# Kernel optimization log

Measured on AMD Instinct MI355X. Metric: run time of the kernel, lower is better.

## Reference

```python
import jax, jax.numpy as jnp
import numpy as np

N = 50000
E = 600000
NODE_DIM = 128
EDGE_DIM = 16
HID = 128


def _tconv(x, src, dst, ea, Wq, bq, Wk, bk, Wv, bv, We, be, Ws, bs, heads, C, concat):
    """PyG TransformerConv (root_weight=True, beta=False), eval mode (no dropout)."""
    n = x.shape[0]
    q = (x @ Wq + bq).reshape(n, heads, C)[dst]          # [E,H,C] query at target
    k = (x @ Wk + bk).reshape(n, heads, C)[src]          # [E,H,C] key at source
    v = (x @ Wv + bv).reshape(n, heads, C)[src]          # [E,H,C] value at source
    e = (ea @ We + be).reshape(-1, heads, C)             # [E,H,C] edge embedding
    k = k + e
    score = (q * k).sum(-1) / jnp.sqrt(jnp.asarray(C, x.dtype))  # [E,H]
    # segment softmax over incoming edges of each target node
    m = jax.ops.segment_max(score, dst, num_segments=n)
    m = jnp.where(jnp.isfinite(m), m, jnp.zeros_like(m))  # nodes w/o in-edges
    ex = jnp.exp(score - m[dst])
    den = jax.ops.segment_sum(ex, dst, num_segments=n)
    alpha = ex / (den[dst] + 1e-16)                       # [E,H]
    msg = (v + e) * alpha[..., None]                      # [E,H,C]
    out = jax.ops.segment_sum(msg, dst, num_segments=n)   # [N,H,C]
    out = out.reshape(n, heads * C) if concat else out.mean(axis=1)
    return out + x @ Ws + bs                              # root skip connection


def setup_inputs() -> dict:
    key = jax.random.key(0)
    ks = jax.random.split(key, 32)
    d = {
        "x": jax.random.normal(ks[0], (N, NODE_DIM), jnp.float32),
        "ei": jax.random.randint(ks[1], (2, E), 0, N, jnp.int32),
        "ea": jax.random.normal(ks[2], (E, EDGE_DIM), jnp.float32),
    }
    H1, C1 = 8, HID // 8
    def w(k, shape):
        return jax.random.normal(k, shape, jnp.float32) * 0.05
    # layer 1: in=NODE_DIM, heads=8, out=HID//8, concat=True
    d["Wq1"] = w(ks[3], (NODE_DIM, H1 * C1)); d["bq1"] = jnp.zeros((H1 * C1,), jnp.float32)
    d["Wk1"] = w(ks[4], (NODE_DIM, H1 * C1)); d["bk1"] = jnp.zeros((H1 * C1,), jnp.float32)
    d["Wv1"] = w(ks[5], (NODE_DIM, H1 * C1)); d["bv1"] = jnp.zeros((H1 * C1,), jnp.float32)
    d["We1"] = w(ks[6], (EDGE_DIM, H1 * C1)); d["be1"] = jnp.zeros((H1 * C1,), jnp.float32)
    d["Ws1"] = w(ks[7], (NODE_DIM, H1 * C1)); d["bs1"] = jnp.zeros((H1 * C1,), jnp.float32)
    # layer 2: in=HID, heads=1, out=HID, concat=False -> skip maps to HID
    d["Wq2"] = w(ks[8], (HID, HID)); d["bq2"] = jnp.zeros((HID,), jnp.float32)
    d["Wk2"] = w(ks[9], (HID, HID)); d["bk2"] = jnp.zeros((HID,), jnp.float32)
    d["Wv2"] = w(ks[10], (HID, HID)); d["bv2"] = jnp.zeros((HID,), jnp.float32)
    d["We2"] = w(ks[11], (EDGE_DIM, HID)); d["be2"] = jnp.zeros((HID,), jnp.float32)
    d["Ws2"] = w(ks[12], (HID, HID)); d["bs2"] = jnp.zeros((HID,), jnp.float32)
    return d


def reference(x, ei, ea,
              Wq1, bq1, Wk1, bk1, Wv1, bv1, We1, be1, Ws1, bs1,
              Wq2, bq2, Wk2, bk2, Wv2, bv2, We2, be2, Ws2, bs2):
    src, dst = ei[0], ei[1]
    h = _tconv(x, src, dst, ea, Wq1, bq1, Wk1, bk1, Wv1, bv1, We1, be1, Ws1, bs1,
               heads=8, C=HID // 8, concat=True)
    h = jax.nn.leaky_relu(h, negative_slope=0.01)
    # dropout is identity in eval mode
    out = _tconv(h, src, dst, ea, Wq2, bq2, Wk2, bk2, Wv2, bv2, We2, be2, Ws2, bs2,
                 heads=1, C=HID, concat=False)
    return out
```

## Files before the change

### kernel.cpp

```cpp
#include <hip/hip_runtime.h>
#include <math.h>

typedef __bf16 bf16x8 __attribute__((ext_vector_type(8)));
typedef float f32x4 __attribute__((ext_vector_type(4)));

__device__ __forceinline__ unsigned short f2bf(float f) {
    unsigned u = __float_as_uint(f);
    return (unsigned short)((u + 0x7fffu + ((u >> 16) & 1u)) >> 16);
}
__device__ __forceinline__ float2 bf2(unsigned u) {
    float2 r;
    r.x = __uint_as_float(u << 16);
    r.y = __uint_as_float(u & 0xffff0000u);
    return r;
}

__global__ __launch_bounds__(256) void convert_x(
    const float* __restrict__ x, unsigned short* __restrict__ xb, int total)
{
    int g = blockIdx.x * blockDim.x + threadIdx.x;
    if (g < total) xb[g] = f2bf(x[g]);
}

__global__ __launch_bounds__(256) void prep_w(
    const float* __restrict__ Wq, const float* __restrict__ bq,
    const float* __restrict__ Wk, const float* __restrict__ bk,
    const float* __restrict__ Wv, const float* __restrict__ bv,
    const float* __restrict__ be,
    const float* __restrict__ Ws, const float* __restrict__ bs,
    const float* __restrict__ We, int H,
    unsigned short* __restrict__ Wt, float* __restrict__ bias)
{
    int g = blockIdx.x * blockDim.x + threadIdx.x;
    const int C = 128 / H;
    if (g < 640) {
        int p = g;
        float b;
        if (p < 256) {
            int cc = 2 * (p >> 2) + (p & 1);
            b = ((p & 2) ? bv[cc] : bk[cc]) + be[cc];
        }
        else if (p < 384) b = bq[p - 256];
        else if (p < 512) b = bs[p - 384];
        else {
            int c2 = p - 512, h = c2 >> 4, kk = c2 & 15;
            b = 0.f;
            if (h < H) for (int i = 0; i < C; ++i) b += bq[h * C + i] * We[kk * 128 + h * C + i];
        }
        bias[p] = b;
    }
    if (g >= 640 * 128) return;
    int p = g >> 7, d = g & 127;
    float w;
    if (p < 256) {
        int cc = 2 * (p >> 2) + (p & 1);
        w = (p & 2) ? Wv[d * 128 + cc] : Wk[d * 128 + cc];
    } else if (p < 384) {
        w = Wq[d * 128 + (p - 256)];
    } else if (p < 512) {
        w = Ws[d * 128 + (p - 384)];
    } else {
        int c2 = p - 512, h = c2 >> 4, kk = c2 & 15;
        w = 0.f;
        if (h < H) for (int i = 0; i < C; ++i) w += Wq[d * 128 + h * C + i] * We[kk * 128 + h * C + i];
    }
    Wt[(size_t)p * 128 + d] = f2bf(w);
}

__global__ __launch_bounds__(256) void gemm_bf16(
    const unsigned short* __restrict__ Xb, int M,
    const unsigned short* __restrict__ Wt, const float* __restrict__ bias,
    unsigned short* __restrict__ P, float* __restrict__ qWe)
{
    __shared__ unsigned short Bs[64][136];
    __shared__ unsigned short tile[4][16][64];
    const int wv = threadIdx.x >> 6, lane = threadIdx.x & 63;
    const int row0 = blockIdx.x * 64 + wv * 16;
    const int n0 = blockIdx.y * 64;
    const int quad = lane >> 4, l16 = lane & 15;

    {
        const uint4* gsrc = (const uint4*)(Wt + (size_t)n0 * 128);
#pragma unroll
        for (int u = 0; u < 4; ++u) {
            int v = threadIdx.x + u * 256;
            int col = v >> 4, k8 = v & 15;
            *(uint4*)(&Bs[col][k8 * 8]) = gsrc[v];
        }
    }
    __syncthreads();

    f32x4 acc[4] = {};
    int mrow = row0 + l16; if (mrow >= M) mrow = M - 1;
    const int kb = quad * 8;
#pragma unroll
    for (int kk = 0; kk < 4; ++kk) {
        bf16x8 a = *(const bf16x8*)(Xb + (size_t)mrow * 128 + kk * 32 + kb);
#pragma unroll
        for (int f = 0; f < 4; ++f) {
            bf16x8 b = *(const bf16x8*)(&Bs[f * 16 + l16][kk * 32 + kb]);
            acc[f] = __builtin_amdgcn_mfma_f32_16x16x32_bf16(a, b, acc[f], 0, 0, 0);
        }
    }
    if (n0 < 512) {
#pragma unroll
        for (int f = 0; f < 4; ++f) {
            float bs = bias[n0 + f * 16 + l16];
#pragma unroll
            for (int r = 0; r < 4; ++r) {
                int row = quad * 4 + r;
                int col = f * 16 + l16;
                tile[wv][row][col ^ ((row & 3) << 4)] = f2bf(acc[f][r] + bs);
            }
        }
        __syncthreads();
        int row = lane >> 2, seg = lane & 3;
        int m = row0 + row;
        if (m < M) {
            const uint4* src = (const uint4*)&tile[wv][row][(seg ^ (row & 3)) << 4];
            uint4* dst = (uint4*)(P + (size_t)m * 512 + n0 + seg * 16);
            dst[0] = src[0];
            dst[1] = src[1];
        }
    } else {
#pragma unroll
        for (int f = 0; f < 4; ++f) {
            int c = n0 + f * 16 + l16;
            float bs = bias[c];
#pragma unroll
            for (int r = 0; r < 4; ++r) {
                int m = row0 + quad * 4 + r;
                if (m < M) qWe[(size_t)m * 128 + (c - 512)] = acc[f][r] + bs;
            }
        }
    }
}

__global__ __launch_bounds__(256) void degree_kernel(
    const int* __restrict__ ei, int* __restrict__ deg, int E)
{
    int e = blockIdx.x * blockDim.x + threadIdx.x;
    if (e < E) atomicAdd(&deg[ei[E + e]], 1);
}

__global__ __launch_bounds__(256) void scan_part1(
    const int* __restrict__ deg, int* __restrict__ partial, int N)
{
    __shared__ int s[256];
    const int t = threadIdx.x;
    const int g = blockIdx.x * 256 + t;
    int v = (g < N) ? deg[g] : 0;
    s[t] = v;
    __syncthreads();
    for (int ofs = 128; ofs > 0; ofs >>= 1) {
        if (t < ofs) s[t] += s[t + ofs];
        __syncthreads();
    }
    if (t == 0) partial[blockIdx.x] = s[0];
}

__global__ __launch_bounds__(256) void scan_part2(
    int* __restrict__ partial)
{
    __shared__ int s[256];
    const int t = threadIdx.x;
    int v = partial[t];
    s[t] = v;
    __syncthreads();
    for (int ofs = 1; ofs < 256; ofs <<= 1) {
        int u = (t >= ofs) ? s[t - ofs] : 0;
        __syncthreads();
        s[t] += u;
        __syncthreads();
    }
    partial[t] = s[t] - v;
}

__global__ __launch_bounds__(256) void scan_part3(
    const int* __restrict__ deg, const int* __restrict__ offs,
    int* __restrict__ rowptr, int* __restrict__ cursor, int N)
{
    __shared__ int s[256];
    const int t = threadIdx.x;
    const int g = blockIdx.x * 256 + t;
    int v = (g < N) ? deg[g] : 0;
    s[t] = v;
    __syncthreads();
    for (int ofs = 1; ofs < 256; ofs <<= 1) {
        int u = (t >= ofs) ? s[t - ofs] : 0;
        __syncthreads();
        s[t] += u;
        __syncthreads();
    }
    const int incl = s[t];
    const int base = offs[blockIdx.x];
    if (g < N) {
        cursor[g] = base + incl - v;
        rowptr[g + 1] = base + incl;
    }
    if (g == 0) rowptr[0] = 0;
}

__global__ __launch_bounds__(256) void scatter_kernel(
    const int* __restrict__ ei, int* __restrict__ cursor,
    int2* __restrict__ csr, int E)
{
    int e = blockIdx.x * blockDim.x + threadIdx.x;
    if (e < E) {
        int pos = atomicAdd(&cursor[ei[E + e]], 1);
        csr[pos] = make_int2(ei[e], e);
    }
}

__global__ __launch_bounds__(256) void fused1_node(
    const unsigned short* __restrict__ P, const float* __restrict__ qWe,
    const float* __restrict__ ea, const float* __restrict__ We1,
    const int2* __restrict__ csr, const int* __restrict__ rowptr,
    unsigned short* __restrict__ h1, int N)
{
    const int lane = threadIdx.x & 63;
    const int node = blockIdx.x * 8 + (threadIdx.x >> 5);
    if (node >= N) return;
    const int l32 = lane & 31;
    const int hbit = lane & 32;
    const int sub4 = l32 & 3;
    const int c0 = l32 * 4;
    const int hsrc = hbit | (l32 & 28);

    const int beg = rowptr[node];
    const int deg = rowptr[node + 1] - beg;

    uint2 su = *(const uint2*)(P + (size_t)node * 512 + 384 + c0);
    float2 ska = bf2(su.x), skb = bf2(su.y);
    if (deg == 0) {
        float o0 = ska.x > 0.f ? ska.x : 0.01f * ska.x;
        float o1 = ska.y > 0.f ? ska.y : 0.01f * ska.y;
        float o2 = skb.x > 0.f ? skb.x : 0.01f * skb.x;
        float o3 = skb.y > 0.f ? skb.y : 0.01f * skb.y;
        uint2 pk;
        pk.x = (unsigned)f2bf(o0) | ((unsigned)f2bf(o1) << 16);
        pk.y = (unsigned)f2bf(o2) | ((unsigned)f2bf(o3) << 16);
        *(uint2*)(h1 + (size_t)node * 128 + c0) = pk;
        return;
    }

    uint2 qu = *(const uint2*)(P + (size_t)node * 512 + 256 + c0);
    float2 qa = bf2(qu.x), qb = bf2(qu.y);
    float4 qw4 = *(const float4*)(qWe + (size_t)node * 128 + c0);

    float4 acc = make_float4(0.f, 0.f, 0.f, 0.f);
    float4 A2  = make_float4(0.f, 0.f, 0.f, 0.f);
    float m = -INFINITY, lden = 0.f;

    int2 se = make_int2(0, 0);
    if (l32 < deg) se = csr[beg + l32];

    for (int blk = 0; blk < deg; blk += 32) {
        if (blk) se = (blk + l32 < deg) ? csr[beg + blk + l32] : make_int2(0, 0);
        const int bcnt = min(32, deg - blk);
        for (int cb = 0; cb < bcnt; cb += 8) {
            const int lim = min(8, bcnt - cb);
            uint4 kv[8]; float4 ea4[8];
#pragma unroll
            for (int i = 0; i < 8; ++i) {
                if (i < lim) {
                    int jc = min(cb + i, bcnt - 1);
                    int sb = __shfl(se.x, hbit | jc, 64);
                    int eb = __shfl(se.y, hbit | jc, 64);
                    kv[i]  = *(const uint4*)(P + (size_t)sb * 512 + l32 * 8);
                    ea4[i] = *(const float4*)(ea + (size_t)eb * 16 + sub4 * 4);
                }
            }
            float s0 = -INFINITY, s1 = -INFINITY;
#pragma unroll
            for (int i = 0; i < 8; ++i) {
                if (i < lim) {
                    float2 ka = bf2(kv[i].x), kb = bf2(kv[i].z);
                    float p = qa.x * ka.x + qa.y * ka.y + qb.x * kb.x + qb.y * kb.y
                            + qw4.x * ea4[i].x + qw4.y * ea4[i].y
                            + qw4.z * ea4[i].z + qw4.w * ea4[i].w;
                    p += __shfl_xor(p, 1, 64);
                    p += __shfl_xor(p, 2, 64);
                    float pv = p * 0.25f;
                    if (sub4 == (i & 3)) { if (i < 4) s0 = pv; else s1 = pv; }
                }
            }
            float cm = fmaxf(s0, s1);
            cm = fmaxf(cm, __shfl_xor(cm, 1, 64));
            cm = fmaxf(cm, __shfl_xor(cm, 2, 64));
            float m_new = fmaxf(m, cm);
            float scale = __expf(m - m_new);
            float e0 = __expf(s0 - m_new);
            float e1 = __expf(s1 - m_new);
            float ds = e0 + e1;
            ds += __shfl_xor(ds, 1, 64);
            ds += __shfl_xor(ds, 2, 64);
            lden = lden * scale + ds;
            acc.x *= scale; acc.y *= scale; acc.z *= scale; acc.w *= scale;
            A2.x  *= scale; A2.y  *= scale; A2.z  *= scale; A2.w  *= scale;
            m = m_new;
#pragma unroll
            for (int i = 0; i < 8; ++i) {
                if (i < lim) {
                    float w = __shfl((i < 4) ? e0 : e1, hsrc | (i & 3), 64);
                    float2 va = bf2(kv[i].y), vb = bf2(kv[i].w);
                    acc.x += w * va.x; acc.y += w * va.y;
                    acc.z += w * vb.x; acc.w += w * vb.y;
                    A2.x += w * ea4[i].x; A2.y += w * ea4[i].y;
                    A2.z += w * ea4[i].z; A2.w += w * ea4[i].w;
                }
            }
        }
    }

    float ex0 = 0.f, ex1 = 0.f, ex2 = 0.f, ex3 = 0.f;
#pragma unroll
    for (int k = 0; k < 16; ++k) {
        float comp = (k & 3) == 0 ? A2.x : (k & 3) == 1 ? A2.y : (k & 3) == 2 ? A2.z : A2.w;
        float ak = __shfl(comp, hsrc | (k >> 2), 64);
        float4 w4 = *(const float4*)(We1 + k * 128 + c0);
        ex0 += ak * w4.x; ex1 += ak * w4.y; ex2 += ak * w4.z; ex3 += ak * w4.w;
    }
    float inv = 1.f / (lden + 1e-16f);
    float o0 = (acc.x + ex0) * inv + ska.x;
    float o1 = (acc.y + ex1) * inv + ska.y;
    float o2 = (acc.z + ex2) * inv + skb.x;
    float o3 = (acc.w + ex3) * inv + skb.y;
    o0 = o0 > 0.f ? o0 : 0.01f * o0;
    o1 = o1 > 0.f ? o1 : 0.01f * o1;
    o2 = o2 > 0.f ? o2 : 0.01f * o2;
    o3 = o3 > 0.f ? o3 : 0.01f * o3;
    uint2 pk;
    pk.x = (unsigned)f2bf(o0) | ((unsigned)f2bf(o1) << 16);
    pk.y = (unsigned)f2bf(o2) | ((unsigned)f2bf(o3) << 16);
    *(uint2*)(h1 + (size_t)node * 128 + c0) = pk;
}

__global__ __launch_bounds__(256) void fused2_node(
    const unsigned short* __restrict__ P, const float* __restrict__ qWe,
    const float* __restrict__ ea, const float* __restrict__ We2,
    const int2* __restrict__ csr, const int* __restrict__ rowptr,
    float* __restrict__ out, int N)
{
    const int lane = threadIdx.x & 63;
    const int node = blockIdx.x * 8 + (threadIdx.x >> 5);
    if (node >= N) return;
    const int l32 = lane & 31;
    const int hbit = lane & 32;
    const int c0 = l32 * 4;
    const int k16 = lane & 15;

    const int beg = rowptr[node];
    const int deg = rowptr[node + 1] - beg;

    uint2 su = *(const uint2*)(P + (size_t)node * 512 + 384 + c0);
    float2 ska = bf2(su.x), skb = bf2(su.y);
    float* outp = out + (size_t)node * 128 + c0;
    if (deg == 0) {
        *(float4*)outp = make_float4(ska.x, ska.y, skb.x, skb.y);
        return;
    }

    uint2 qu = *(const uint2*)(P + (size_t)node * 512 + 256 + c0);
    float2 qa = bf2(qu.x), qb = bf2(qu.y);
    float qw = qWe[(size_t)node * 128 + k16];

    float4 acc = make_float4(0.f, 0.f, 0.f, 0.f);
    float accA = 0.f;
    float m = -INFINITY, lden = 0.f;

    int2 se = make_int2(0, 0);
    if (l32 < deg) se = csr[beg + l32];

    for (int blk = 0; blk < deg; blk += 32) {
        if (blk) se = (blk + l32 < deg) ? csr[beg + blk + l32] : make_int2(0, 0);
        const int bcnt = min(32, deg - blk);
        for (int cb = 0; cb < bcnt; cb += 8) {
            const int lim = min(8, bcnt - cb);
            uint4 kv[8]; float eav[8];
#pragma unroll
            for (int i = 0; i < 8; ++i) {
                if (i < lim) {
                    int jc = min(cb + i, bcnt - 1);
                    int sb = __shfl(se.x, hbit | jc, 64);
                    int eb = __shfl(se.y, hbit | jc, 64);
                    kv[i]  = *(const uint4*)(P + (size_t)sb * 512 + l32 * 8);
                    eav[i] = ea[(size_t)eb * 16 + k16];
                }
            }
            float my_s = -INFINITY;
#pragma unroll
            for (int i = 0; i < 8; ++i) {
                if (i < lim) {
                    float2 ka = bf2(kv[i].x), kb = bf2(kv[i].z);
                    float p = qa.x * ka.x + qa.y * ka.y + qb.x * kb.x + qb.y * kb.y
                            + 0.5f * qw * eav[i];
                    p += __shfl_xor(p, 1, 64);
                    p += __shfl_xor(p, 2, 64);
                    p += __shfl_xor(p, 4, 64);
                    p += __shfl_xor(p, 8, 64);
                    p += __shfl_xor(p, 16, 64);
                    if (l32 == i) my_s = p * 0.08838834764831845f;
                }
            }
            float cm = my_s;
#pragma unroll
            for (int mk = 1; mk < 32; mk <<= 1) cm = fmaxf(cm, __shfl_xor(cm, mk, 64));
            float m_new = fmaxf(m, cm);
            float scale = __expf(m - m_new);
            float ew = __expf(my_s - m_new);
            float ds = ew;
#pragma unroll
            for (int mk = 1; mk < 32; mk <<= 1) ds += __shfl_xor(ds, mk, 64);
            lden = lden * scale + ds;
            acc.x *= scale; acc.y *= scale; acc.z *= scale; acc.w *= scale;
            accA *= scale;
            m = m_new;
#pragma unroll
            for (int i = 0; i < 8; ++i) {
                if (i < lim) {
                    float w = __shfl(ew, hbit | i, 64);
                    float2 va = bf2(kv[i].y), vb = bf2(kv[i].w);
                    acc.x += w * va.x; acc.y += w * va.y;
                    acc.z += w * vb.x; acc.w += w * vb.y;
                    accA += w * eav[i];
                }
            }
        }
    }

    float ex0 = 0.f, ex1 = 0.f, ex2 = 0.f, ex3 = 0.f;
#pragma unroll
    for (int k = 0; k < 16; ++k) {
        float ak = __shfl(accA, hbit | k, 64);
        float4 w4 = *(const float4*)(We2 + k * 128 + c0);
        ex0 += ak * w4.x; ex1 += ak * w4.y; ex2 += ak * w4.z; ex3 += ak * w4.w;
    }
    float inv = 1.f / (lden + 1e-16f);
    float4 o;
    o.x = (acc.x + ex0) * inv + ska.x;
    o.y = (acc.y + ex1) * inv + ska.y;
    o.z = (acc.z + ex2) * inv + skb.x;
    o.w = (acc.w + ex3) * inv + skb.y;
    *(float4*)outp = o;
}

extern "C" void kernel_launch(void* const* d_in, const int* in_sizes, int n_in,
                              void* d_out, int out_size, void* d_ws, size_t ws_size,
                              hipStream_t stream)
{
    const float* x  = (const float*)d_in[0];
    const int*   ei = (const int*)d_in[1];
    const float* ea = (const float*)d_in[2];
    const float *Wq1 = (const float*)d_in[3],  *bq1 = (const float*)d_in[4];
    const float *Wk1 = (const float*)d_in[5],  *bk1 = (const float*)d_in[6];
    const float *Wv1 = (const float*)d_in[7],  *bv1 = (const float*)d_in[8];
    const float *We1 = (const float*)d_in[9],  *be1 = (const float*)d_in[10];
    const float *Ws1 = (const float*)d_in[11], *bs1 = (const float*)d_in[12];
    const float *Wq2 = (const float*)d_in[13], *bq2 = (const float*)d_in[14];
    const float *Wk2 = (const float*)d_in[15], *bk2 = (const float*)d_in[16];
    const float *Wv2 = (const float*)d_in[17], *bv2 = (const float*)d_in[18];
    const float *We2 = (const float*)d_in[19], *be2 = (const float*)d_in[20];
    const float *Ws2 = (const float*)d_in[21], *bs2 = (const float*)d_in[22];

    const int N = in_sizes[0] / 128;
    const int E = in_sizes[1] / 2;

    char* ws = (char*)d_ws;
    size_t off = 0;
    auto alloc = [&](size_t bytes) -> void* {
        void* p = ws + off;
        off = (off + bytes + 255) & ~(size_t)255;
        return p;
    };
    unsigned short* xb  = (unsigned short*)alloc((size_t)N * 128 * 2);
    unsigned short* P   = (unsigned short*)alloc((size_t)N * 512 * 2);
    unsigned short* h1b = (unsigned short*)alloc((size_t)N * 128 * 2);
    unsigned short* Wt1 = (unsigned short*)alloc((size_t)640 * 128 * 2);
    unsigned short* Wt2 = (unsigned short*)alloc((size_t)640 * 128 * 2);
    float* bias1 = (float*)alloc(640 * 4);
    float* bias2 = (float*)alloc(640 * 4);
    float* qWe   = (float*)alloc((size_t)N * 128 * 4);
    int*  deg    = (int*)alloc((size_t)N * 4);
    int*  rowptr = (int*)alloc((size_t)(N + 1) * 4);
    int*  cursor = (int*)alloc((size_t)N * 4);
    int*  partial= (int*)alloc(256 * 4);
    int2* csr    = (int2*)alloc((size_t)E * 8);

    dim3 gemm_grid1((N + 63) / 64, 10);
    dim3 gemm_grid2((N + 63) / 64, 9);
    const int tn = N * 128;
    const int node_blocks = (N + 7) / 8;
    const int prep_blocks = (640 * 128 + 255) / 256;
    const int scan_blocks = (N + 255) / 256;

    convert_x<<<(tn + 255) / 256, 256, 0, stream>>>(x, xb, tn);
    prep_w<<<prep_blocks, 256, 0, stream>>>(Wq1, bq1, Wk1, bk1, Wv1, bv1, be1, Ws1, bs1, We1, 8, Wt1, bias1);
    prep_w<<<prep_blocks, 256, 0, stream>>>(Wq2, bq2, Wk2, bk2, Wv2, bv2, be2, Ws2, bs2, We2, 1, Wt2, bias2);

    hipMemsetAsync(deg, 0, (size_t)N * 4, stream);
    hipMemsetAsync(partial, 0, 256 * 4, stream);
    degree_kernel<<<(E + 255) / 256, 256, 0, stream>>>(ei, deg, E);
    scan_part1<<<scan_blocks, 256, 0, stream>>>(deg, partial, N);
    scan_part2<<<1, 256, 0, stream>>>(partial);
    scan_part3<<<scan_blocks, 256, 0, stream>>>(deg, partial, rowptr, cursor, N);
    scatter_kernel<<<(E + 255) / 256, 256, 0, stream>>>(ei, cursor, csr, E);

    gemm_bf16<<<gemm_grid1, 256, 0, stream>>>(xb, N, Wt1, bias1, P, qWe);
    fused1_node<<<node_blocks, 256, 0, stream>>>(P, qWe, ea, We1, csr, rowptr, h1b, N);

    gemm_bf16<<<gemm_grid2, 256, 0, stream>>>(h1b, N, Wt2, bias2, P, qWe);
    fused2_node<<<node_blocks, 256, 0, stream>>>(P, qWe, ea, We2, csr, rowptr, (float*)d_out, N);
}
```

Before: 498.4 us.

## Use 16 lanes per node in fused attention kernels, 8 channels per lane

Both fused node kernels now map each destination node to 16 lanes instead of 32, with every lane handling 8 channels through two 16-byte loads. The aim is fewer shuffle-reduction steps per edge, wider vector loads, and twice as many nodes per block so uneven degrees leave fewer lanes idle. In exchange, each lane holds more registers for key/value and edge-feature tiles. The edge batch per iteration also shrinks from 8 to 4, which lowers memory-level parallelism per node.

```diff
diff --git a/kernel.cpp b/kernel.cpp
--- a/kernel.cpp
+++ b/kernel.cpp
@@ -219,121 +219,159 @@
     unsigned short* __restrict__ h1, int N)
 {
     const int lane = threadIdx.x & 63;
-    const int node = blockIdx.x * 8 + (threadIdx.x >> 5);
+    const int node = blockIdx.x * 16 + (threadIdx.x >> 4);
     if (node >= N) return;
-    const int l32 = lane & 31;
-    const int hbit = lane & 32;
-    const int sub4 = l32 & 3;
-    const int c0 = l32 * 4;
-    const int hsrc = hbit | (l32 & 28);
+    const int l16 = lane & 15;
+    const int qbit = lane & 48;
+    const int pbit = lane & 62;
+    const int odd  = lane & 1;
+    const int c0 = l16 * 8;
 
     const int beg = rowptr[node];
     const int deg = rowptr[node + 1] - beg;
 
-    uint2 su = *(const uint2*)(P + (size_t)node * 512 + 384 + c0);
-    float2 ska = bf2(su.x), skb = bf2(su.y);
+    uint4 su = *(const uint4*)(P + (size_t)node * 512 + 384 + c0);
+    float2 sk0 = bf2(su.x), sk1 = bf2(su.y), sk2 = bf2(su.z), sk3 = bf2(su.w);
     if (deg == 0) {
-        float o0 = ska.x > 0.f ? ska.x : 0.01f * ska.x;
-        float o1 = ska.y > 0.f ? ska.y : 0.01f * ska.y;
-        float o2 = skb.x > 0.f ? skb.x : 0.01f * skb.x;
-        float o3 = skb.y > 0.f ? skb.y : 0.01f * skb.y;
-        uint2 pk;
+        float o0 = sk0.x > 0.f ? sk0.x : 0.01f * sk0.x;
+        float o1 = sk0.y > 0.f ? sk0.y : 0.01f * sk0.y;
+        float o2 = sk1.x > 0.f ? sk1.x : 0.01f * sk1.x;
+        float o3 = sk1.y > 0.f ? sk1.y : 0.01f * sk1.y;
+        float o4 = sk2.x > 0.f ? sk2.x : 0.01f * sk2.x;
+        float o5 = sk2.y > 0.f ? sk2.y : 0.01f * sk2.y;
+        float o6 = sk3.x > 0.f ? sk3.x : 0.01f * sk3.x;
+        float o7 = sk3.y > 0.f ? sk3.y : 0.01f * sk3.y;
+        uint4 pk;
         pk.x = (unsigned)f2bf(o0) | ((unsigned)f2bf(o1) << 16);
         pk.y = (unsigned)f2bf(o2) | ((unsigned)f2bf(o3) << 16);
-        *(uint2*)(h1 + (size_t)node * 128 + c0) = pk;
+        pk.z = (unsigned)f2bf(o4) | ((unsigned)f2bf(o5) << 16);
+        pk.w = (unsigned)f2bf(o6) | ((unsigned)f2bf(o7) << 16);
+        *(uint4*)(h1 + (size_t)node * 128 + c0) = pk;
         return;
     }
 
-    uint2 qu = *(const uint2*)(P + (size_t)node * 512 + 256 + c0);
-    float2 qa = bf2(qu.x), qb = bf2(qu.y);
-    float4 qw4 = *(const float4*)(qWe + (size_t)node * 128 + c0);
-
-    float4 acc = make_float4(0.f, 0.f, 0.f, 0.f);
-    float4 A2  = make_float4(0.f, 0.f, 0.f, 0.f);
+    uint4 qu = *(const uint4*)(P + (size_t)node * 512 + 256 + c0);
+    float2 q0 = bf2(qu.x), q1 = bf2(qu.y), q2 = bf2(qu.z), q3 = bf2(qu.w);
+    float4 qwA = *(const float4*)(qWe + (size_t)node * 128 + c0);
+    float4 qwB = *(const float4*)(qWe + (size_t)node * 128 + c0 + 4);
+
+    float4 acA = make_float4(0.f, 0.f, 0.f, 0.f);
+    float4 acB = make_float4(0.f, 0.f, 0.f, 0.f);
+    float4 A2a = make_float4(0.f, 0.f, 0.f, 0.f);
+    float4 A2b = make_float4(0.f, 0.f, 0.f, 0.f);
     float m = -INFINITY, lden = 0.f;
 
     int2 se = make_int2(0, 0);
-    if (l32 < deg) se = csr[beg + l32];
-
-    for (int blk = 0; blk < deg; blk += 32) {
-        if (blk) se = (blk + l32 < deg) ? csr[beg + blk + l32] : make_int2(0, 0);
-        const int bcnt = min(32, deg - blk);
-        for (int cb = 0; cb < bcnt; cb += 8) {
-            const int lim = min(8, bcnt - cb);
-            uint4 kv[8]; float4 ea4[8];
-#pragma unroll
-            for (int i = 0; i < 8; ++i) {
+    if (l16 < deg) se = csr[beg + l16];
+
+    for (int blk = 0; blk < deg; blk += 16) {
+        if (blk) se = (blk + l16 < deg) ? csr[beg + blk + l16] : make_int2(0, 0);
+        const int bcnt = min(16, deg - blk);
+        for (int cb = 0; cb < bcnt; cb += 4) {
+            const int lim = min(4, bcnt - cb);
+            uint4 kva[4], kvb[4]; float4 eaA[4], eaB[4];
+#pragma unroll
+            for (int i = 0; i < 4; ++i) {
                 if (i < lim) {
                     int jc = min(cb + i, bcnt - 1);
-                    int sb = __shfl(se.x, hbit | jc, 64);
-                    int eb = __shfl(se.y, hbit | jc, 64);
-                    kv[i]  = *(const uint4*)(P + (size_t)sb * 512 + l32 * 8);
-                    ea4[i] = *(const float4*)(ea + (size_t)eb * 16 + sub4 * 4);
+                    int sb = __shfl(se.x, qbit | jc, 64);
+                    int eb = __shfl(se.y, qbit | jc, 64);
+                    const unsigned short* kp = P + (size_t)sb * 512 + l16 * 16;
+                    kva[i] = *(const uint4*)(kp);
+                    kvb[i] = *(const uint4*)(kp + 8);
+                    const float* ep = ea + (size_t)eb * 16 + odd * 8;
+                    eaA[i] = *(const float4*)(ep);
+                    eaB[i] = *(const float4*)(ep + 4);
                 }
             }
             float s0 = -INFINITY, s1 = -INFINITY;
 #pragma unroll
-            for (int i = 0; i < 8; ++i) {
+            for (int i = 0; i < 4; ++i) {
                 if (i < lim) {
-                    float2 ka = bf2(kv[i].x), kb = bf2(kv[i].z);
-                    float p = qa.x * ka.x + qa.y * ka.y + qb.x * kb.x + qb.y * kb.y
-                            + qw4.x * ea4[i].x + qw4.y * ea4[i].y
-                            + qw4.z * ea4[i].z + qw4.w * ea4[i].w;
+                    float2 ka = bf2(kva[i].x), kb = bf2(kva[i].z);
+                    float2 kc = bf2(kvb[i].x), kd = bf2(kvb[i].z);
+                    float p = q0.x * ka.x + q0.y * ka.y + q1.x * kb.x + q1.y * kb.y
+                            + q2.x * kc.x + q2.y * kc.y + q3.x * kd.x + q3.y * kd.y
+                            + qwA.x * eaA[i].x + qwA.y * eaA[i].y
+                            + qwA.z * eaA[i].z + qwA.w * eaA[i].w
+                            + qwB.x * eaB[i].x + qwB.y * eaB[i].y
+                            + qwB.z * eaB[i].z + qwB.w * eaB[i].w;
                     p += __shfl_xor(p, 1, 64);
-                    p += __shfl_xor(p, 2, 64);
                     float pv = p * 0.25f;
-                    if (sub4 == (i & 3)) { if (i < 4) s0 = pv; else s1 = pv; }
+                    if (odd == (i & 1)) { if (i < 2) s0 = pv; else s1 = pv; }
                 }
             }
             float cm = fmaxf(s0, s1);
             cm = fmaxf(cm, __shfl_xor(cm, 1, 64));
-            cm = fmaxf(cm, __shfl_xor(cm, 2, 64));
             float m_new = fmaxf(m, cm);
             float scale = __expf(m - m_new);
             float e0 = __expf(s0 - m_new);
             float e1 = __expf(s1 - m_new);
             float ds = e0 + e1;
             ds += __shfl_xor(ds, 1, 64);
-            ds += __shfl_xor(ds, 2, 64);
             lden = lden * scale + ds;
-            acc.x *= scale; acc.y *= scale; acc.z *= scale; acc.w *= scale;
-            A2.x  *= scale; A2.y  *= scale; A2.z  *= scale; A2.w  *= scale;
+            acA.x *= scale; acA.y *= scale; acA.z *= scale; acA.w *= scale;
+            acB.x *= scale; acB.y *= scale; acB.z *= scale; acB.w *= scale;
+            A2a.x *= scale; A2a.y *= scale; A2a.z *= scale; A2a.w *= scale;
+            A2b.x *= scale; A2b.y *= scale; A2b.z *= scale; A2b.w *= scale;
             m = m_new;
 #pragma unroll
-            for (int i = 0; i < 8; ++i) {
+            for (int i = 0; i < 4; ++i) {
                 if (i < lim) {
-                    float w = __shfl((i < 4) ? e0 : e1, hsrc | (i & 3), 64);
-                    float2 va = bf2(kv[i].y), vb = bf2(kv[i].w);
-                    acc.x += w * va.x; acc.y += w * va.y;
-                    acc.z += w * vb.x; acc.w += w * vb.y;
-                    A2.x += w * ea4[i].x; A2.y += w * ea4[i].y;
-                    A2.z += w * ea4[i].z; A2.w += w * ea4[i].w;
+                    float w = __shfl((i < 2) ? e0 : e1, pbit | (i & 1), 64);
+                    float2 va = bf2(kva[i].y), vb = bf2(kva[i].w);
+                    float2 vc = bf2(kvb[i].y), vd = bf2(kvb[i].w);
+                    acA.x += w * va.x; acA.y += w * va.y;
+                    acA.z += w * vb.x; acA.w += w * vb.y;
+                    acB.x += w * vc.x; acB.y += w * vc.y;
+                    acB.z += w * vd.x; acB.w += w * vd.y;
+                    A2a.x += w * eaA[i].x; A2a.y += w * eaA[i].y;
+                    A2a.z += w * eaA[i].z; A2a.w += w * eaA[i].w;
+                    A2b.x += w * eaB[i].x; A2b.y += w * eaB[i].y;
+                    A2b.z += w * eaB[i].z; A2b.w += w * eaB[i].w;
                 }
             }
         }
     }
 
     float ex0 = 0.f, ex1 = 0.f, ex2 = 0.f, ex3 = 0.f;
+    float ex4 = 0.f, ex5 = 0.f, ex6 = 0.f, ex7 = 0.f;
 #pragma unroll
     for (int k = 0; k < 16; ++k) {
-        float comp = (k & 3) == 0 ? A2.x : (k & 3) == 1 ? A2.y : (k & 3) == 2 ? A2.z : A2.w;
-        float ak = __shfl(comp, hsrc | (k >> 2), 64);
-        float4 w4 = *(const float4*)(We1 + k * 128 + c0);
-        ex0 += ak * w4.x; ex1 += ak * w4.y; ex2 += ak * w4.z; ex3 += ak * w4.w;
+        float comp = (k & 7) == 0 ? A2a.x : (k & 7) == 1 ? A2a.y :
+                     (k & 7) == 2 ? A2a.z : (k & 7) == 3 ? A2a.w :
+                     (k & 7) == 4 ? A2b.x : (k & 7) == 5 ? A2b.y :
+                     (k & 7) == 6 ? A2b.z : A2b.w;
+        float ak = __shfl(comp, pbit | (k >> 3), 64);
+        const float* wp = We1 + k * 128 + c0;
+        float4 w4a = *(const float4*)(wp);
+        float4 w4b = *(const float4*)(wp + 4);
+        ex0 += ak * w4a.x; ex1 += ak * w4a.y; ex2 += ak * w4a.z; ex3 += ak * w4a.w;
+        ex4 += ak * w4b.x; ex5 += ak * w4b.y; ex6 += ak * w4b.z; ex7 += ak * w4b.w;
     }
     float inv = 1.f / (lden + 1e-16f);
-    float o0 = (acc.x + ex0) * inv + ska.x;
-    float o1 = (acc.y + ex1) * inv + ska.y;
-    float o2 = (acc.z + ex2) * inv + skb.x;
-    float o3 = (acc.w + ex3) * inv + skb.y;
+    float o0 = (acA.x + ex0) * inv + sk0.x;
+    float o1 = (acA.y + ex1) * inv + sk0.y;
+    float o2 = (acA.z + ex2) * inv + sk1.x;
+    float o3 = (acA.w + ex3) * inv + sk1.y;
+    float o4 = (acB.x + ex4) * inv + sk2.x;
+    float o5 = (acB.y + ex5) * inv + sk2.y;
+    float o6 = (acB.z + ex6) * inv + sk3.x;
+    float o7 = (acB.w + ex7) * inv + sk3.y;
     o0 = o0 > 0.f ? o0 : 0.01f * o0;
     o1 = o1 > 0.f ? o1 : 0.01f * o1;
     o2 = o2 > 0.f ? o2 : 0.01f * o2;
     o3 = o3 > 0.f ? o3 : 0.01f * o3;
-    uint2 pk;
+    o4 = o4 > 0.f ? o4 : 0.01f * o4;
+    o5 = o5 > 0.f ? o5 : 0.01f * o5;
+    o6 = o6 > 0.f ? o6 : 0.01f * o6;
+    o7 = o7 > 0.f ? o7 : 0.01f * o7;
+    uint4 pk;
     pk.x = (unsigned)f2bf(o0) | ((unsigned)f2bf(o1) << 16);
     pk.y = (unsigned)f2bf(o2) | ((unsigned)f2bf(o3) << 16);
-    *(uint2*)(h1 + (size_t)node * 128 + c0) = pk;
+    pk.z = (unsigned)f2bf(o4) | ((unsigned)f2bf(o5) << 16);
+    pk.w = (unsigned)f2bf(o6) | ((unsigned)f2bf(o7) << 16);
+    *(uint4*)(h1 + (size_t)node * 128 + c0) = pk;
 }
 
 __global__ __launch_bounds__(256) void fused2_node(
@@ -343,86 +381,94 @@
     float* __restrict__ out, int N)
 {
     const int lane = threadIdx.x & 63;
-    const int node = blockIdx.x * 8 + (threadIdx.x >> 5);
+    const int node = blockIdx.x * 16 + (threadIdx.x >> 4);
     if (node >= N) return;
-    const int l32 = lane & 31;
-    const int hbit = lane & 32;
-    const int c0 = l32 * 4;
-    const int k16 = lane & 15;
+    const int l16 = lane & 15;
+    const int qbit = lane & 48;
+    const int c0 = l16 * 8;
 
     const int beg = rowptr[node];
     const int deg = rowptr[node + 1] - beg;
 
-    uint2 su = *(const uint2*)(P + (size_t)node * 512 + 384 + c0);
-    float2 ska = bf2(su.x), skb = bf2(su.y);
+    uint4 su = *(const uint4*)(P + (size_t)node * 512 + 384 + c0);
+    float2 sk0 = bf2(su.x), sk1 = bf2(su.y), sk2 = bf2(su.z), sk3 = bf2(su.w);
     float* outp = out + (size_t)node * 128 + c0;
     if (deg == 0) {
-        *(float4*)outp = make_float4(ska.x, ska.y, skb.x, skb.y);
+        *(float4*)outp = make_float4(sk0.x, sk0.y, sk1.x, sk1.y);
+        *(float4*)(outp + 4) = make_float4(sk2.x, sk2.y, sk3.x, sk3.y);
         return;
     }
 
-    uint2 qu = *(const uint2*)(P + (size_t)node * 512 + 256 + c0);
-    float2 qa = bf2(qu.x), qb = bf2(qu.y);
-    float qw = qWe[(size_t)node * 128 + k16];
-
-    float4 acc = make_float4(0.f, 0.f, 0.f, 0.f);
+    uint4 qu = *(const uint4*)(P + (size_t)node * 512 + 256 + c0);
+    float2 q0 = bf2(qu.x), q1 = bf2(qu.y), q2 = bf2(qu.z), q3 = bf2(qu.w);
+    float qw = qWe[(size_t)node * 128 + l16];
+
+    float4 acA = make_float4(0.f, 0.f, 0.f, 0.f);
+    float4 acB = make_float4(0.f, 0.f, 0.f, 0.f);
     float accA = 0.f;
     float m = -INFINITY, lden = 0.f;
 
     int2 se = make_int2(0, 0);
-    if (l32 < deg) se = csr[beg + l32];
-
-    for (int blk = 0; blk < deg; blk += 32) {
-        if (blk) se = (blk + l32 < deg) ? csr[beg + blk + l32] : make_int2(0, 0);
-        const int bcnt = min(32, deg - blk);
-        for (int cb = 0; cb < bcnt; cb += 8) {
-            const int lim = min(8, bcnt - cb);
-            uint4 kv[8]; float eav[8];
-#pragma unroll
-            for (int i = 0; i < 8; ++i) {
+    if (l16 < deg) se = csr[beg + l16];
+
+    for (int blk = 0; blk < deg; blk += 16) {
+        if (blk) se = (blk + l16 < deg) ? csr[beg + blk + l16] : make_int2(0, 0);
+        const int bcnt = min(16, deg - blk);
+        for (int cb = 0; cb < bcnt; cb += 4) {
+            const int lim = min(4, bcnt - cb);
+            uint4 kva[4], kvb[4]; float eav[4];
+#pragma unroll
+            for (int i = 0; i < 4; ++i) {
                 if (i < lim) {
                     int jc = min(cb + i, bcnt - 1);
-                    int sb = __shfl(se.x, hbit | jc, 64);
-                    int eb = __shfl(se.y, hbit | jc, 64);
-                    kv[i]  = *(const uint4*)(P + (size_t)sb * 512 + l32 * 8);
-                    eav[i] = ea[(size_t)eb * 16 + k16];
+                    int sb = __shfl(se.x, qbit | jc, 64);
+                    int eb = __shfl(se.y, qbit | jc, 64);
+                    const unsigned short* kp = P + (size_t)sb * 512 + l16 * 16;
+                    kva[i] = *(const uint4*)(kp);
+                    kvb[i] = *(const uint4*)(kp + 8);
+                    eav[i] = ea[(size_t)eb * 16 + l16];
                 }
             }
             float my_s = -INFINITY;
 #pragma unroll
-            for (int i = 0; i < 8; ++i) {
+            for (int i = 0; i < 4; ++i) {
                 if (i < lim) {
-                    float2 ka = bf2(kv[i].x), kb = bf2(kv[i].z);
-                    float p = qa.x * ka.x + qa.y * ka.y + qb.x * kb.x + qb.y * kb.y
-                            + 0.5f * qw * eav[i];
+                    float2 ka = bf2(kva[i].x), kb = bf2(kva[i].z);
+                    float2 kc = bf2(kvb[i].x), kd = bf2(kvb[i].z);
+                    float p = q0.x * ka.x + q0.y * ka.y + q1.x * kb.x + q1.y * kb.y
+                            + q2.x * kc.x + q2.y * kc.y + q3.x * kd.x + q3.y * kd.y
+                            + qw * eav[i];
                     p += __shfl_xor(p, 1, 64);
                     p += __shfl_xor(p, 2, 64);
                     p += __shfl_xor(p, 4, 64);
                     p += __shfl_xor(p, 8, 64);
-                    p += __shfl_xor(p, 16, 64);
-                    if (l32 == i) my_s = p * 0.08838834764831845f;
+                    if (l16 == i) my_s = p * 0.08838834764831845f;
                 }
             }
             float cm = my_s;
 #pragma unroll
-            for (int mk = 1; mk < 32; mk <<= 1) cm = fmaxf(cm, __shfl_xor(cm, mk, 64));
+            for (int mk = 1; mk < 16; mk <<= 1) cm = fmaxf(cm, __shfl_xor(cm, mk, 64));
             float m_new = fmaxf(m, cm);
             float scale = __expf(m - m_new);
             float ew = __expf(my_s - m_new);
             float ds = ew;
 #pragma unroll
-            for (int mk = 1; mk < 32; mk <<= 1) ds += __shfl_xor(ds, mk, 64);
+            for (int mk = 1; mk < 16; mk <<= 1) ds += __shfl_xor(ds, mk, 64);
             lden = lden * scale + ds;
-            acc.x *= scale; acc.y *= scale; acc.z *= scale; acc.w *= scale;
+            acA.x *= scale; acA.y *= scale; acA.z *= scale; acA.w *= scale;
+            acB.x *= scale; acB.y *= scale; acB.z *= scale; acB.w *= scale;
             accA *= scale;
             m = m_new;
 #pragma unroll
-            for (int i = 0; i < 8; ++i) {
+            for (int i = 0; i < 4; ++i) {
                 if (i < lim) {
-                    float w = __shfl(ew, hbit | i, 64);
-                    float2 va = bf2(kv[i].y), vb = bf2(kv[i].w);
-                    acc.x += w * va.x; acc.y += w * va.y;
-                    acc.z += w * vb.x; acc.w += w * vb.y;
+                    float w = __shfl(ew, qbit | i, 64);
+                    float2 va = bf2(kva[i].y), vb = bf2(kva[i].w);
+                    float2 vc = bf2(kvb[i].y), vd = bf2(kvb[i].w);
+                    acA.x += w * va.x; acA.y += w * va.y;
+                    acA.z += w * vb.x; acA.w += w * vb.y;
+                    acB.x += w * vc.x; acB.y += w * vc.y;
+                    acB.z += w * vd.x; acB.w += w * vd.y;
                     accA += w * eav[i];
                 }
             }
@@ -430,19 +476,28 @@
     }
 
     float ex0 = 0.f, ex1 = 0.f, ex2 = 0.f, ex3 = 0.f;
+    float ex4 = 0.f, ex5 = 0.f, ex6 = 0.f, ex7 = 0.f;
 #pragma unroll
     for (int k = 0; k < 16; ++k) {
-        float ak = __shfl(accA, hbit | k, 64);
-        float4 w4 = *(const float4*)(We2 + k * 128 + c0);
-        ex0 += ak * w4.x; ex1 += ak * w4.y; ex2 += ak * w4.z; ex3 += ak * w4.w;
+        float ak = __shfl(accA, qbit | k, 64);
+        const float* wp = We2 + k * 128 + c0;
+        float4 w4a = *(const float4*)(wp);
+        float4 w4b = *(const float4*)(wp + 4);
+        ex0 += ak * w4a.x; ex1 += ak * w4a.y; ex2 += ak * w4a.z; ex3 += ak * w4a.w;
+        ex4 += ak * w4b.x; ex5 += ak * w4b.y; ex6 += ak * w4b.z; ex7 += ak * w4b.w;
     }
     float inv = 1.f / (lden + 1e-16f);
-    float4 o;
-    o.x = (acc.x + ex0) * inv + ska.x;
-    o.y = (acc.y + ex1) * inv + ska.y;
-    o.z = (acc.z + ex2) * inv + skb.x;
-    o.w = (acc.w + ex3) * inv + skb.y;
-    *(float4*)outp = o;
+    float4 oA, oB;
+    oA.x = (acA.x + ex0) * inv + sk0.x;
+    oA.y = (acA.y + ex1) * inv + sk0.y;
+    oA.z = (acA.z + ex2) * inv + sk1.x;
+    oA.w = (acA.w + ex3) * inv + sk1.y;
+    oB.x = (acB.x + ex4) * inv + sk2.x;
+    oB.y = (acB.y + ex5) * inv + sk2.y;
+    oB.z = (acB.z + ex6) * inv + sk3.x;
+    oB.w = (acB.w + ex7) * inv + sk3.y;
+    *(float4*)outp = oA;
+    *(float4*)(outp + 4) = oB;
 }
 
 extern "C" void kernel_launch(void* const* d_in, const int* in_sizes, int n_in,
@@ -490,7 +545,7 @@
     dim3 gemm_grid1((N + 63) / 64, 10);
     dim3 gemm_grid2((N + 63) / 64, 9);
     const int tn = N * 128;
-    const int node_blocks = (N + 7) / 8;
+    const int node_blocks = (N + 15) / 16;
     const int prep_blocks = (640 * 128 + 255) / 256;
     const int scan_blocks = (N + 255) / 256;
 
```

Result: faster. 477.8 us (-4.1%).
